# Kernel optimization log

Measured on AMD Instinct MI355X. Metric: run time of the kernel, lower is better.

The kernel has to match this reference:

```python
import jax, jax.numpy as jnp
import numpy as np

B, L, C = 2, 2048, 1024
H, HD = 16, 64
MAX_SCALE_MUL = float(np.log(100.0))
SCALE = 1.0  # attn_l2_norm=True -> scale is 1


def setup_inputs() -> dict:
    key = jax.random.key(0)
    ks = jax.random.split(key, 6)
    x = jax.random.normal(ks[0], (B, L, C), dtype=jnp.float32)
    attn_bias = jax.random.normal(ks[1], (1, 1, L, L), dtype=jnp.float32)
    w_qkv = jax.random.normal(ks[2], (3 * C, C), dtype=jnp.float32) * (1.0 / np.sqrt(C))
    q_bias = jnp.zeros((C,), dtype=jnp.float32)
    v_bias = jnp.zeros((C,), dtype=jnp.float32)
    scale_mul = jnp.full((1, H, 1, 1), np.log(4.0), dtype=jnp.float32)  # scale_mul_1H11
    w_proj = jax.random.normal(ks[3], (C, C), dtype=jnp.float32) * (1.0 / np.sqrt(C))
    b_proj = jnp.zeros((C,), dtype=jnp.float32)
    return {"x": x, "attn_bias": attn_bias, "w_qkv": w_qkv, "q_bias": q_bias,
            "v_bias": v_bias, "scale_mul": scale_mul, "w_proj": w_proj, "b_proj": b_proj}


def reference(x, attn_bias, w_qkv, q_bias, v_bias, scale_mul, w_proj, b_proj):
    # qkv projection with concatenated bias (q_bias, zeros, v_bias)
    bias = jnp.concatenate([q_bias, jnp.zeros_like(q_bias), v_bias])  # [3C]
    qkv = jnp.einsum('blc,dc->bld', x, w_qkv) + bias                  # [B,L,3C]
    qkv = qkv.reshape(B, L, 3, H, HD).transpose(2, 0, 3, 1, 4)        # [3,B,H,L,HD]
    q, k, v = qkv[0], qkv[1], qkv[2]
    # attn_l2_norm path: L2-normalize q,k; q scaled by exp(clamped scale_mul)
    sm = jnp.exp(jnp.minimum(scale_mul, MAX_SCALE_MUL))               # [1,H,1,1]
    q = q / jnp.linalg.norm(q, axis=-1, keepdims=True) * sm
    k = k / jnp.linalg.norm(k, axis=-1, keepdims=True)
    # slow_attn: scaled scores + bias, softmax, weighted sum
    attn = jnp.einsum('bhld,bhmd->bhlm', q * SCALE, k) + attn_bias    # [B,H,L,L]
    p = jax.nn.softmax(attn, axis=-1)
    oup = jnp.einsum('bhlm,bhmd->bhld', p, v)                         # [B,H,L,HD]
    oup = oup.transpose(0, 2, 1, 3).reshape(B, L, C)
    return jnp.einsum('blc,dc->bld', oup, w_proj) + b_proj
```

## Files before the change

### kernel.cpp

```cpp
#include <hip/hip_runtime.h>
#include <cstdint>
#include <cstddef>
#include <math.h>

typedef __attribute__((ext_vector_type(8))) __bf16 bf16x8;
typedef __attribute__((ext_vector_type(4))) __bf16 bf16x4;
typedef __attribute__((ext_vector_type(4))) float f32x4;
typedef __attribute__((ext_vector_type(4))) unsigned int u32x4;

#define AS1 __attribute__((address_space(1)))
#define AS3 __attribute__((address_space(3)))

#define LOG2E 1.4426950408889634f

__device__ __forceinline__ void gld16(void* lds_uniform, const void* gaddr) {
  __builtin_amdgcn_global_load_lds((const AS1 unsigned int*)gaddr,
                                   (AS3 unsigned int*)lds_uniform, 16, 0, 0);
}

__global__ __launch_bounds__(256)
void prep_kernel(const float* __restrict__ x, const float* __restrict__ wqkv,
                 const float* __restrict__ wproj, const float* __restrict__ bias,
                 __bf16* __restrict__ xb, __bf16* __restrict__ wqkvb,
                 __bf16* __restrict__ wprojb, __bf16* __restrict__ btr) {
  __shared__ __bf16 T[32][264];
  const int b = blockIdx.x;
  const int tid = threadIdx.x;
  if (b < 2048) {
    const float* src; __bf16* dst; int fb;
    if (b < 1024)      { src = x;     dst = xb;     fb = b; }
    else if (b < 1792) { src = wqkv;  dst = wqkvb;  fb = b - 1024; }
    else               { src = wproj; dst = wprojb; fb = b - 1792; }
#pragma unroll
    for (int q = 0; q < 4; ++q) {
      const size_t i = ((size_t)fb * 1024 + q * 256 + tid) * 4;
      const float4 v = *(const float4*)(src + i);
      bf16x4 o;
      o[0] = (__bf16)v.x; o[1] = (__bf16)v.y; o[2] = (__bf16)v.z; o[3] = (__bf16)v.w;
      *(bf16x4*)(dst + i) = o;
    }
    return;
  }
  const int bb = b - 2048;
  const int rb = bb >> 3, cg = bb & 7;
  const float* src = bias + (size_t)(rb * 32) * 2048 + cg * 256;
#pragma unroll
  for (int i = 0; i < 8; ++i) {
    const int u = i * 256 + tid;
    const int r = u >> 6, c4 = (u & 63) * 4;
    const float4 v = *(const float4*)(src + (size_t)r * 2048 + c4);
    T[r][c4 + 0] = (__bf16)(v.x * LOG2E);
    T[r][c4 + 1] = (__bf16)(v.y * LOG2E);
    T[r][c4 + 2] = (__bf16)(v.z * LOG2E);
    T[r][c4 + 3] = (__bf16)(v.w * LOG2E);
  }
  __syncthreads();
  const int ktl = tid >> 6;
  const int lane = tid & 63, g = lane >> 4, cc = lane & 15;
#pragma unroll
  for (int sub = 0; sub < 2; ++sub) {
    __bf16 outv[16];
#pragma unroll
    for (int v = 0; v < 16; ++v) {
      const int ni = v >> 2, j = v & 3;
      outv[v] = T[sub * 16 + cc][ktl * 64 + ni * 16 + g * 4 + j];
    }
    __bf16* dst = btr + ((size_t)(((rb * 2 + sub) * 32) + cg * 4 + ktl) * 64 + lane) * 16;
    *(bf16x8*)(dst) = *(bf16x8*)(outv);
    *(bf16x8*)(dst + 8) = *(bf16x8*)(outv + 8);
  }
}

__global__ __launch_bounds__(256, 3)
void gemm_qkv_kernel(const __bf16* __restrict__ A, const __bf16* __restrict__ B,
                     const float* __restrict__ q_bias, const float* __restrict__ v_bias,
                     const float* __restrict__ scale_mul,
                     __bf16* __restrict__ qb, __bf16* __restrict__ ktp, __bf16* __restrict__ vtp) {
  __shared__ __attribute__((aligned(16))) __bf16 As[2][128 * 32];
  __shared__ __attribute__((aligned(16))) __bf16 Bs[2][128 * 32];
  const int tid = threadIdx.x;
  const int w = tid >> 6, lane = tid & 63;
  const int bid = blockIdx.x;
  const int swz = (bid & 7) * 96 + (bid >> 3);
  const int m0 = (swz / 24) * 128, n0 = (swz % 24) * 128;
  const int wm = (w >> 1) * 64, wn = (w & 1) * 64;
  const int c = lane & 15, g = lane >> 4;
  f32x4 acc[4][4];
#pragma unroll
  for (int i = 0; i < 4; ++i)
#pragma unroll
    for (int j = 0; j < 4; ++j) acc[i][j] = (f32x4)(0.0f);

  const int r_row = lane >> 2;
  const int r_col = (lane & 3) * 16;
  const char* Abase = (const char*)A + (size_t)m0 * 2048;
  const char* Bbase = (const char*)B + (size_t)n0 * 2048;

  for (int kt = 0; kt < 1024; kt += 64) {
#pragma unroll
    for (int ks = 0; ks < 2; ++ks)
#pragma unroll
      for (int s = 0; s < 2; ++s) {
        const int R = w * 2 + s;
        const int row = R * 16 + r_row;
        gld16((char*)&As[ks][0] + R * 1024, Abase + (size_t)row * 2048 + kt * 2 + ks * 64 + r_col);
        gld16((char*)&Bs[ks][0] + R * 1024, Bbase + (size_t)row * 2048 + kt * 2 + ks * 64 + r_col);
      }
    __syncthreads();
#pragma unroll
    for (int ks = 0; ks < 2; ++ks) {
      bf16x8 af[4], bfr[4];
#pragma unroll
      for (int i = 0; i < 4; ++i) {
        af[i]  = *(const bf16x8*)((const char*)&As[ks][0] + (wm + i * 16 + c) * 64 + g * 16);
        bfr[i] = *(const bf16x8*)((const char*)&Bs[ks][0] + (wn + i * 16 + c) * 64 + g * 16);
      }
#pragma unroll
      for (int ni = 0; ni < 4; ++ni)
#pragma unroll
        for (int mi = 0; mi < 4; ++mi)
          acc[ni][mi] = __builtin_amdgcn_mfma_f32_16x16x32_bf16(bfr[ni], af[mi], acc[ni][mi], 0, 0, 0);
    }
    __syncthreads();
  }

  const int nbase = n0 + wn;
  const int which = nbase >> 10;
  const int h = (nbase >> 6) & 15;
  float smh = 1.0f;
  if (which == 0) smh = __expf(fminf(scale_mul[h], 4.605170185988091f)) * LOG2E;
  float4 cb[4];
#pragma unroll
  for (int ni = 0; ni < 4; ++ni) {
    if (which == 0)      cb[ni] = *(const float4*)(q_bias + nbase + ni * 16 + 4 * g);
    else if (which == 2) cb[ni] = *(const float4*)(v_bias + nbase - 2048 + ni * 16 + 4 * g);
    else                 cb[ni] = make_float4(0.f, 0.f, 0.f, 0.f);
  }
  const int mrow0 = m0 + wm;
  const int b2 = mrow0 >> 11;
  const int lpos0 = mrow0 & 2047;
  __bf16* kt_tile = ktp + (size_t)(b2 * 16 + h) * 131072 + (size_t)(lpos0 >> 6) * 4096;
  __bf16* dst_q = qb + ((size_t)((b2 * 16 + h) * 2048 + lpos0)) * 64;
  __bf16* vtile = vtp + ((size_t)((b2 * 16 + h) * 32) + (lpos0 >> 6)) * 4096;
  __bf16* Ls = (__bf16*)((char*)&As[0][0] + w * 8192);

#pragma unroll
  for (int mi = 0; mi < 4; ++mi) {
    float v[4][4];
#pragma unroll
    for (int ni = 0; ni < 4; ++ni) {
      v[ni][0] = acc[ni][mi][0] + cb[ni].x;
      v[ni][1] = acc[ni][mi][1] + cb[ni].y;
      v[ni][2] = acc[ni][mi][2] + cb[ni].z;
      v[ni][3] = acc[ni][mi][3] + cb[ni].w;
    }
    const int key = mi * 16 + c;
    if (which == 2) {
      const int ks2 = mi >> 1;
      const int gg  = ((mi & 1) << 1) | (c >> 3);
      const int e   = c & 7;
      __bf16* basep = Ls + ks2 * 2048 + gg * 8 + e;
#pragma unroll
      for (int ni = 0; ni < 4; ++ni)
#pragma unroll
        for (int j = 0; j < 4; ++j)
          basep[ni * 512 + (4 * g + j) * 32] = (__bf16)v[ni][j];
    } else {
      float ss = 0.0f;
#pragma unroll
      for (int ni = 0; ni < 4; ++ni)
#pragma unroll
        for (int j = 0; j < 4; ++j) ss += v[ni][j] * v[ni][j];
      ss += __shfl_xor(ss, 16, 64);
      ss += __shfl_xor(ss, 32, 64);
      const float sc = rsqrtf(ss) * smh;
      if (which == 1) {
#pragma unroll
        for (int ni = 0; ni < 4; ++ni) {
          bf16x4 pk;
          pk[0] = (__bf16)(v[ni][0] * sc); pk[1] = (__bf16)(v[ni][1] * sc);
          pk[2] = (__bf16)(v[ni][2] * sc); pk[3] = (__bf16)(v[ni][3] * sc);
          *(bf16x4*)(kt_tile + (ni >> 1) * 2048 + key * 32 + (ni & 1) * 16 + 4 * g) = pk;
        }
      } else {
        __bf16* drow = dst_q + (size_t)key * 64;
#pragma unroll
        for (int ni = 0; ni < 4; ++ni) {
          bf16x4 pk;
          pk[0] = (__bf16)(v[ni][0] * sc); pk[1] = (__bf16)(v[ni][1] * sc);
          pk[2] = (__bf16)(v[ni][2] * sc); pk[3] = (__bf16)(v[ni][3] * sc);
          *(bf16x4*)(drow + ni * 16 + 4 * g) = pk;
        }
      }
    }
  }
  if (which == 2) {
#pragma unroll
    for (int r = 0; r < 8; ++r) {
      const int o = r * 512 + lane * 8;
      *(bf16x8*)(vtile + o) = *(const bf16x8*)(Ls + o);
    }
  }
}

#define STAGE(t, b) {                                                          \
  const char* _ks = kp + (size_t)(t) * 8192 + w * 1024 + sl16;                 \
  const char* _vs = vp + (size_t)(t) * 8192 + w * 1024 + sl16;                 \
  gld16(&Kb[b][w * 1024], _ks);                                                \
  gld16(&Vb[b][w * 1024], _vs);                                                \
}

#define BAV(ni, j) ((ni * 4 + j < 8) ? bA0[(ni * 4 + j) & 7] : bA1[(ni * 4 + j) & 7])

#define COMPUTE(t, b) {                                                        \
  bf16x8 kf[4][2];                                                             \
  _Pragma("unroll")                                                            \
  for (int ni = 0; ni < 4; ++ni)                                               \
    _Pragma("unroll")                                                          \
    for (int ks = 0; ks < 2; ++ks)                                             \
      kf[ni][ks] = *(const bf16x8*)(&Kb[b][0] + ks * 4096 + (ni * 16 + c) * 64 + gsw16); \
  f32x4 sacc[4];                                                               \
  __builtin_amdgcn_s_setprio(1);                                               \
  _Pragma("unroll")                                                            \
  for (int ni = 0; ni < 4; ++ni) {                                             \
    f32x4 s_ = __builtin_amdgcn_mfma_f32_16x16x32_bf16(kf[ni][0], qf[0], (f32x4)(0.0f), 0, 0, 0); \
    sacc[ni] = __builtin_amdgcn_mfma_f32_16x16x32_bf16(kf[ni][1], qf[1], s_, 0, 0, 0); \
  }                                                                            \
  __builtin_amdgcn_s_setprio(0);                                               \
  unsigned qp[4][2];                                                           \
  _Pragma("unroll")                                                            \
  for (int ni = 0; ni < 4; ++ni) {                                             \
    const float p0 = __builtin_amdgcn_exp2f(sacc[ni][0] + (float)BAV(ni, 0));  \
    const float p1 = __builtin_amdgcn_exp2f(sacc[ni][1] + (float)BAV(ni, 1));  \
    const float p2 = __builtin_amdgcn_exp2f(sacc[ni][2] + (float)BAV(ni, 2));  \
    const float p3 = __builtin_amdgcn_exp2f(sacc[ni][3] + (float)BAV(ni, 3));  \
    lsum += (p0 + p1) + (p2 + p3);                                             \
    asm("v_cvt_pk_bf16_f32 %0, %1, %2" : "=v"(qp[ni][0]) : "v"(p0), "v"(p1));  \
    asm("v_cvt_pk_bf16_f32 %0, %1, %2" : "=v"(qp[ni][1]) : "v"(p2), "v"(p3));  \
  }                                                                            \
  {  \
    const int _tn = ((t) < 31) ? ((t) + 1) : 31;                               \
    const char* _bb = bp + (size_t)_tn * 2048 + lane * 32;                     \
    bA0 = *(const bf16x8*)_bb;                                                 \
    bA1 = *(const bf16x8*)(_bb + 16);                                          \
  }                                                                            \
  bf16x8 pf[2];                                                                \
  _Pragma("unroll")                                                            \
  for (int ks = 0; ks < 2; ++ks) {                                             \
    unsigned x0 = qp[2 * ks][0], x1 = qp[2 * ks][1];                           \
    unsigned y0 = qp[2 * ks + 1][0], y1 = qp[2 * ks + 1][1];                   \
    asm("v_permlane32_swap_b32 %0, %1" : "+v"(x0), "+v"(y0));                  \
    asm("v_permlane16_swap_b32 %0, %1" : "+v"(x0), "+v"(y0));                  \
    asm("v_permlane32_swap_b32 %0, %1" : "+v"(x1), "+v"(y1));                  \
    asm("v_permlane16_swap_b32 %0, %1" : "+v"(x1), "+v"(y1));                  \
    u32x4 t_; t_[0] = x0; t_[1] = x1; t_[2] = y0; t_[3] = y1;                  \
    pf[ks] = __builtin_bit_cast(bf16x8, t_);                                   \
  }                                                                            \
  __builtin_amdgcn_s_setprio(1);                                               \
  _Pragma("unroll")                                                            \
  for (int ni = 0; ni < 4; ++ni) {                                             \
    const bf16x8 v0 = *(const bf16x8*)(&Vb[b][0] + 0 * 4096 + ni * 1024 + c * 64 + gsw16); \
    const bf16x8 v1 = *(const bf16x8*)(&Vb[b][0] + 1 * 4096 + ni * 1024 + c * 64 + gsw16); \
    oacc[ni] = __builtin_amdgcn_mfma_f32_16x16x32_bf16(pf[0], v0, oacc[ni], 0, 0, 0); \
    oacc[ni] = __builtin_amdgcn_mfma_f32_16x16x32_bf16(pf[1], v1, oacc[ni], 0, 0, 0); \
  }                                                                            \
  __builtin_amdgcn_s_setprio(0);                                               \
}

__global__ __launch_bounds__(512, 4)
void attn_kernel(const __bf16* __restrict__ qb, const __bf16* __restrict__ ktp,
                 const __bf16* __restrict__ vtp, const __bf16* __restrict__ btr,
                 __bf16* __restrict__ oupb) {
  __shared__ __attribute__((aligned(16))) char Kb[2][8192];
  __shared__ __attribute__((aligned(16))) char Vb[2][8192];
  const int tid = threadIdx.x, w = tid >> 6, lane = tid & 63;
  const int c = lane & 15, g = lane >> 4;
  const int sl16 = (lane ^ ((lane >> 3) & 3)) * 16;
  const int gsw16 = (g ^ ((c >> 1) & 3)) * 16;
  const int idx = blockIdx.x;
  const int bh = idx & 31, rb = idx >> 5;
  const __bf16* qh = qb + (size_t)bh * (2048 * 64);
  const char* kp = (const char*)ktp + (size_t)bh * (32 * 8192);
  const char* vp = (const char*)vtp + (size_t)bh * (32 * 8192);
  const char* bp = (const char*)btr + (size_t)(rb * 8 + w) * 65536;
  const int q0 = rb * 128 + w * 16;
  const int b2 = bh >> 4, h = bh & 15;

  bf16x8 qf[2];
#pragma unroll
  for (int ks = 0; ks < 2; ++ks)
    qf[ks] = *(const bf16x8*)(qh + (size_t)(q0 + c) * 64 + ks * 32 + g * 8);

  bf16x8 bA0 = *(const bf16x8*)(bp + lane * 32);
  bf16x8 bA1 = *(const bf16x8*)(bp + lane * 32 + 16);

  f32x4 oacc[4];
  float lsum = 0.0f;
#pragma unroll
  for (int ni = 0; ni < 4; ++ni) oacc[ni] = (f32x4)(0.0f);

  STAGE(0, 0);
  __syncthreads();
#pragma unroll 1
  for (int tt = 0; tt < 32; tt += 2) {
    if (tt + 1 < 32) STAGE(tt + 1, 1);
    COMPUTE(tt, 0);
    __syncthreads();
    if (tt + 2 < 32) STAGE(tt + 2, 0);
    COMPUTE(tt + 1, 1);
    __syncthreads();
  }

  float l = lsum;
  l += __shfl_xor(l, 16, 64);
  l += __shfl_xor(l, 32, 64);
#pragma unroll
  for (int j = 0; j < 4; ++j) {
    const float lr = __shfl(l, g * 4 + j, 64);
    const float inv = 1.0f / lr;
    const int qrow = q0 + g * 4 + j;
    __bf16* orow = oupb + ((size_t)(b2 * 2048 + qrow) * 16 + h) * 64;
#pragma unroll
    for (int ni = 0; ni < 4; ++ni)
      orow[ni * 16 + c] = (__bf16)(oacc[ni][j] * inv);
  }
}

__global__ __launch_bounds__(256, 2)
void gemm_proj_kernel(const __bf16* __restrict__ A, const __bf16* __restrict__ B,
                      const float* __restrict__ b_proj, float* __restrict__ out) {
  __shared__ __attribute__((aligned(16))) __bf16 As[2][64 * 32];
  __shared__ __attribute__((aligned(16))) __bf16 Bs[2][128 * 32];
  const int tid = threadIdx.x;
  const int w = tid >> 6, lane = tid & 63;
  const int c = lane & 15, g = lane >> 4;
  const int m0 = blockIdx.y * 64, n0 = blockIdx.x * 128;
  const int wm = (w >> 1) * 32, wn = (w & 1) * 64;
  f32x4 acc[2][4];
#pragma unroll
  for (int i = 0; i < 2; ++i)
#pragma unroll
    for (int j = 0; j < 4; ++j) acc[i][j] = (f32x4)(0.0f);

  const int r_row = lane >> 2;
  const int r_col = (lane & 3) * 16;
  const char* Abase = (const char*)A + (size_t)m0 * 2048;
  const char* Bbase = (const char*)B + (size_t)n0 * 2048;

  for (int kt = 0; kt < 1024; kt += 64) {
#pragma unroll
    for (int ks = 0; ks < 2; ++ks) {
      {
        const int row = w * 16 + r_row;
        gld16((char*)&As[ks][0] + w * 1024, Abase + (size_t)row * 2048 + kt * 2 + ks * 64 + r_col);
      }
#pragma unroll
      for (int s = 0; s < 2; ++s) {
        const int R = w * 2 + s;
        const int row = R * 16 + r_row;
        gld16((char*)&Bs[ks][0] + R * 1024, Bbase + (size_t)row * 2048 + kt * 2 + ks * 64 + r_col);
      }
    }
    __syncthreads();
#pragma unroll
    for (int ks = 0; ks < 2; ++ks) {
      bf16x8 af[2], bfr[4];
#pragma unroll
      for (int i = 0; i < 2; ++i)
        af[i] = *(const bf16x8*)((const char*)&As[ks][0] + (wm + i * 16 + c) * 64 + g * 16);
#pragma unroll
      for (int i = 0; i < 4; ++i)
        bfr[i] = *(const bf16x8*)((const char*)&Bs[ks][0] + (wn + i * 16 + c) * 64 + g * 16);
#pragma unroll
      for (int mi = 0; mi < 2; ++mi)
#pragma unroll
        for (int ni = 0; ni < 4; ++ni)
          acc[mi][ni] = __builtin_amdgcn_mfma_f32_16x16x32_bf16(af[mi], bfr[ni], acc[mi][ni], 0, 0, 0);
    }
    __syncthreads();
  }

  float cbias[4];
#pragma unroll
  for (int ni = 0; ni < 4; ++ni) cbias[ni] = b_proj[n0 + wn + ni * 16 + c];
#pragma unroll
  for (int mi = 0; mi < 2; ++mi)
#pragma unroll
    for (int j = 0; j < 4; ++j) {
      const int m = m0 + wm + mi * 16 + g * 4 + j;
      float* orow = out + (size_t)m * 1024 + n0 + wn;
#pragma unroll
      for (int ni = 0; ni < 4; ++ni)
        orow[ni * 16 + c] = acc[mi][ni][j] + cbias[ni];
    }
}

extern "C" void kernel_launch(void* const* d_in, const int* in_sizes, int n_in,
                              void* d_out, int out_size, void* d_ws, size_t ws_size,
                              hipStream_t stream) {
  const float* x         = (const float*)d_in[0];
  const float* attn_bias = (const float*)d_in[1];
  const float* w_qkv     = (const float*)d_in[2];
  const float* q_bias    = (const float*)d_in[3];
  const float* v_bias    = (const float*)d_in[4];
  const float* scale_mul = (const float*)d_in[5];
  const float* w_proj    = (const float*)d_in[6];
  const float* b_proj    = (const float*)d_in[7];
  float* out = (float*)d_out;

  __bf16* xb     = (__bf16*)d_ws;
  __bf16* wqkvb  = xb + 4194304;
  __bf16* wprojb = wqkvb + 3145728;
  __bf16* qb     = wprojb + 1048576;
  __bf16* ktp    = qb + 4194304;
  __bf16* vtp    = ktp + 4194304;
  __bf16* btr    = vtp + 4194304;
  __bf16* oupb   = xb;

  prep_kernel<<<2560, 256, 0, stream>>>(x, w_qkv, w_proj, attn_bias, xb, wqkvb, wprojb, btr);
  gemm_qkv_kernel<<<768, 256, 0, stream>>>(xb, wqkvb, q_bias, v_bias, scale_mul,
                                           qb, ktp, vtp);
  attn_kernel<<<512, 512, 0, stream>>>(qb, ktp, vtp, btr, oupb);
  gemm_proj_kernel<<<dim3(8, 64), 256, 0, stream>>>(oupb, wprojb, b_proj, out);
}
```

Baseline: 201.1 us.

## Double-buffer LDS k-tiles in QKV and projection GEMMs to overlap loads

Both GEMM kernels previously loaded a 64-wide k chunk into two LDS halves, synchronized, computed, then synchronized again, so global loads and MFMA work were serialized. They now use 32-wide k steps with ping-pong buffers: the next tile's global-to-LDS load is issued before computing on the current buffer, with one barrier per step. This aims to hide global load latency behind compute. In exchange it doubles the number of loop iterations and barriers per GEMM.

Measured after the change: 204.5 us. No clear change (+1.7%).

```diff
diff --git a/kernel.cpp b/kernel.cpp
--- a/kernel.cpp
+++ b/kernel.cpp
@@ -69,6 +69,16 @@
     *(bf16x8*)(dst) = *(bf16x8*)(outv);
     *(bf16x8*)(dst + 8) = *(bf16x8*)(outv + 8);
   }
+}
+
+#define QSTAGE(kt, b) {                                                        \
+  _Pragma("unroll")                                                            \
+  for (int s = 0; s < 2; ++s) {                                                \
+    const int R = w * 2 + s;                                                   \
+    const int row = R * 16 + r_row;                                            \
+    gld16((char*)&As[b][0] + R * 1024, Abase + (size_t)row * 2048 + (kt) * 2 + r_col); \
+    gld16((char*)&Bs[b][0] + R * 1024, Bbase + (size_t)row * 2048 + (kt) * 2 + r_col); \
+  }                                                                            \
 }
 
 __global__ __launch_bounds__(256, 3)
@@ -96,32 +106,25 @@
   const char* Abase = (const char*)A + (size_t)m0 * 2048;
   const char* Bbase = (const char*)B + (size_t)n0 * 2048;
 
-  for (int kt = 0; kt < 1024; kt += 64) {
-#pragma unroll
-    for (int ks = 0; ks < 2; ++ks)
-#pragma unroll
-      for (int s = 0; s < 2; ++s) {
-        const int R = w * 2 + s;
-        const int row = R * 16 + r_row;
-        gld16((char*)&As[ks][0] + R * 1024, Abase + (size_t)row * 2048 + kt * 2 + ks * 64 + r_col);
-        gld16((char*)&Bs[ks][0] + R * 1024, Bbase + (size_t)row * 2048 + kt * 2 + ks * 64 + r_col);
-      }
+  QSTAGE(0, 0);
+  __syncthreads();
+  int cur = 0;
+#pragma unroll 1
+  for (int kt = 0; kt < 1024; kt += 32) {
+    if (kt + 32 < 1024) QSTAGE(kt + 32, cur ^ 1);
+    bf16x8 af[4], bfr[4];
+#pragma unroll
+    for (int i = 0; i < 4; ++i) {
+      af[i]  = *(const bf16x8*)((const char*)&As[cur][0] + (wm + i * 16 + c) * 64 + g * 16);
+      bfr[i] = *(const bf16x8*)((const char*)&Bs[cur][0] + (wn + i * 16 + c) * 64 + g * 16);
+    }
+#pragma unroll
+    for (int ni = 0; ni < 4; ++ni)
+#pragma unroll
+      for (int mi = 0; mi < 4; ++mi)
+        acc[ni][mi] = __builtin_amdgcn_mfma_f32_16x16x32_bf16(bfr[ni], af[mi], acc[ni][mi], 0, 0, 0);
     __syncthreads();
-#pragma unroll
-    for (int ks = 0; ks < 2; ++ks) {
-      bf16x8 af[4], bfr[4];
-#pragma unroll
-      for (int i = 0; i < 4; ++i) {
-        af[i]  = *(const bf16x8*)((const char*)&As[ks][0] + (wm + i * 16 + c) * 64 + g * 16);
-        bfr[i] = *(const bf16x8*)((const char*)&Bs[ks][0] + (wn + i * 16 + c) * 64 + g * 16);
-      }
-#pragma unroll
-      for (int ni = 0; ni < 4; ++ni)
-#pragma unroll
-        for (int mi = 0; mi < 4; ++mi)
-          acc[ni][mi] = __builtin_amdgcn_mfma_f32_16x16x32_bf16(bfr[ni], af[mi], acc[ni][mi], 0, 0, 0);
-    }
-    __syncthreads();
+    cur ^= 1;
   }
 
   const int nbase = n0 + wn;
@@ -326,6 +329,19 @@
   }
 }
 
+#define PSTAGE(kt, b) {                                                        \
+  {                                                                            \
+    const int row = w * 16 + r_row;                                            \
+    gld16((char*)&As[b][0] + w * 1024, Abase + (size_t)row * 2048 + (kt) * 2 + r_col); \
+  }                                                                            \
+  _Pragma("unroll")                                                            \
+  for (int s = 0; s < 2; ++s) {                                                \
+    const int R = w * 2 + s;                                                   \
+    const int row = R * 16 + r_row;                                            \
+    gld16((char*)&Bs[b][0] + R * 1024, Bbase + (size_t)row * 2048 + (kt) * 2 + r_col); \
+  }                                                                            \
+}
+
 __global__ __launch_bounds__(256, 2)
 void gemm_proj_kernel(const __bf16* __restrict__ A, const __bf16* __restrict__ B,
                       const float* __restrict__ b_proj, float* __restrict__ out) {
@@ -347,37 +363,26 @@
   const char* Abase = (const char*)A + (size_t)m0 * 2048;
   const char* Bbase = (const char*)B + (size_t)n0 * 2048;
 
-  for (int kt = 0; kt < 1024; kt += 64) {
-#pragma unroll
-    for (int ks = 0; ks < 2; ++ks) {
-      {
-        const int row = w * 16 + r_row;
-        gld16((char*)&As[ks][0] + w * 1024, Abase + (size_t)row * 2048 + kt * 2 + ks * 64 + r_col);
-      }
-#pragma unroll
-      for (int s = 0; s < 2; ++s) {
-        const int R = w * 2 + s;
-        const int row = R * 16 + r_row;
-        gld16((char*)&Bs[ks][0] + R * 1024, Bbase + (size_t)row * 2048 + kt * 2 + ks * 64 + r_col);
-      }
-    }
+  PSTAGE(0, 0);
+  __syncthreads();
+  int cur = 0;
+#pragma unroll 1
+  for (int kt = 0; kt < 1024; kt += 32) {
+    if (kt + 32 < 1024) PSTAGE(kt + 32, cur ^ 1);
+    bf16x8 af[2], bfr[4];
+#pragma unroll
+    for (int i = 0; i < 2; ++i)
+      af[i] = *(const bf16x8*)((const char*)&As[cur][0] + (wm + i * 16 + c) * 64 + g * 16);
+#pragma unroll
+    for (int i = 0; i < 4; ++i)
+      bfr[i] = *(const bf16x8*)((const char*)&Bs[cur][0] + (wn + i * 16 + c) * 64 + g * 16);
+#pragma unroll
+    for (int mi = 0; mi < 2; ++mi)
+#pragma unroll
+      for (int ni = 0; ni < 4; ++ni)
+        acc[mi][ni] = __builtin_amdgcn_mfma_f32_16x16x32_bf16(af[mi], bfr[ni], acc[mi][ni], 0, 0, 0);
     __syncthreads();
-#pragma unroll
-    for (int ks = 0; ks < 2; ++ks) {
-      bf16x8 af[2], bfr[4];
-#pragma unroll
-      for (int i = 0; i < 2; ++i)
-        af[i] = *(const bf16x8*)((const char*)&As[ks][0] + (wm + i * 16 + c) * 64 + g * 16);
-#pragma unroll
-      for (int i = 0; i < 4; ++i)
-        bfr[i] = *(const bf16x8*)((const char*)&Bs[ks][0] + (wn + i * 16 + c) * 64 + g * 16);
-#pragma unroll
-      for (int mi = 0; mi < 2; ++mi)
-#pragma unroll
-        for (int ni = 0; ni < 4; ++ni)
-          acc[mi][ni] = __builtin_amdgcn_mfma_f32_16x16x32_bf16(af[mi], bfr[ni], acc[mi][ni], 0, 0, 0);
-    }
-    __syncthreads();
+    cur ^= 1;
   }
 
   float cbias[4];
```
